# Optimization experiments

Measured on AMD Instinct MI355X. Metric: run time of the kernel, lower is better.

Reference implementation:

```python
import jax, jax.numpy as jnp
import numpy as np

NUM_EMBEDDINGS = 1024
EMBEDDING_DIM = 256
COMMITMENT_COST = 0.25


def setup_inputs() -> dict:
    key = jax.random.key(0)
    k1, k2 = jax.random.split(key)
    x = jax.random.normal(k1, (64, EMBEDDING_DIM, 32, 32), dtype=jnp.float32)
    # nn.init.uniform_(weight, -1/K, 1/K)
    lim = 1.0 / NUM_EMBEDDINGS
    codebook = jax.random.uniform(k2, (NUM_EMBEDDINGS, EMBEDDING_DIM),
                                  dtype=jnp.float32, minval=-lim, maxval=lim)
    return {"x": x, "codebook": codebook}


def reference(x, codebook):
    # x: [B, D, H, W], codebook: [K, D]
    B, D, H, W = x.shape
    xf = jnp.moveaxis(x, 1, -1).reshape(-1, D)  # [N, D], N = B*H*W
    # Squared L2 distances via expansion (same argmin as vector_norm of diff),
    # avoids materializing the [N, K, D] difference tensor.
    d2 = (
        jnp.sum(xf * xf, axis=-1, keepdims=True)          # [N, 1]
        - 2.0 * jnp.einsum("nd,kd->nk", xf, codebook)      # [N, K]
        + jnp.sum(codebook * codebook, axis=-1)            # [K]
    )
    idx = jnp.argmin(d2, axis=-1)                          # [N]
    q = codebook[idx].reshape(B, H, W, D)                  # gather + reshape
    q = jnp.moveaxis(q, -1, 1)                             # [B, D, H, W]

    codebook_loss = jnp.mean((jax.lax.stop_gradient(x) - q) ** 2)
    commitment_loss = COMMITMENT_COST * jnp.mean((x - jax.lax.stop_gradient(q)) ** 2)
    vq_loss = codebook_loss + commitment_loss

    # Straight-through estimator
    quantized = x + jax.lax.stop_gradient(q - x)
    return quantized, vq_loss
```

## Files before the change

### kernel.cpp

```cpp
#include <hip/hip_runtime.h>

#define BATCH 64
#define DIM 256
#define HW 1024
#define N_POS 65536
#define K_CODES 1024
#define NTOT 16777216

typedef __bf16 bf16x8 __attribute__((ext_vector_type(8)));
typedef float f32x4 __attribute__((ext_vector_type(4)));

__device__ inline unsigned short f2bf(float f) {
    unsigned int u = __builtin_bit_cast(unsigned int, f);
    unsigned int r = u + 0x7FFFu + ((u >> 16) & 1u);
    return (unsigned short)(r >> 16);
}
__device__ inline float bf2f(unsigned short u) {
    unsigned int x = ((unsigned int)u) << 16;
    return __builtin_bit_cast(float, x);
}

__global__ void cbprep_kernel(const float* __restrict__ cb, unsigned short* __restrict__ cbt,
                              float* __restrict__ cnorm) {
    const int wv = threadIdx.x >> 6, lane = threadIdx.x & 63;
    const int k = blockIdx.x * 4 + wv;
    const float4 v = *reinterpret_cast<const float4*>(cb + (size_t)k * DIM + lane * 4);
    ushort4 pk;
    pk.x = f2bf(v.x); pk.y = f2bf(v.y); pk.z = f2bf(v.z); pk.w = f2bf(v.w);
    *reinterpret_cast<ushort4*>(cbt + (size_t)k * DIM + lane * 4) = pk;
    const float f0 = bf2f(pk.x), f1 = bf2f(pk.y), f2 = bf2f(pk.z), f3 = bf2f(pk.w);
    float s = f0 * f0 + f1 * f1 + f2 * f2 + f3 * f3;
    #pragma unroll
    for (int off = 32; off; off >>= 1) s += __shfl_xor(s, off);
    if (lane == 0) cnorm[k] = 0.5f * s;
}

__global__ __launch_bounds__(256) void transpose_kernel(
        const float* __restrict__ x, unsigned short* __restrict__ xt) {
    __shared__ unsigned char ts[64 * 512];
    const int tid = threadIdx.x;
    const int b  = blockIdx.x >> 4;
    const int p0 = (blockIdx.x & 15) << 6;
    const float* xb = x + (size_t)b * (DIM * HW) + p0;
    const int p4 = tid & 15;
    const int dh = tid >> 4;
    #pragma unroll
    for (int dp = 0; dp < 8; ++dp) {
        const int d0 = dp * 32 + dh * 2;
        const float4 v0 = *reinterpret_cast<const float4*>(xb + (size_t)d0 * HW + p4 * 4);
        const float4 v1 = *reinterpret_cast<const float4*>(xb + (size_t)(d0 + 1) * HW + p4 * 4);
        const float a0[4] = {v0.x, v0.y, v0.z, v0.w};
        const float a1[4] = {v1.x, v1.y, v1.z, v1.w};
        #pragma unroll
        for (int e = 0; e < 4; ++e) {
            const int p = p4 * 4 + e;
            const unsigned int pk = (unsigned int)f2bf(a0[e]) | ((unsigned int)f2bf(a1[e]) << 16);
            const int col = (d0 * 2) ^ ((p & 7) << 4);
            *reinterpret_cast<unsigned int*>(&ts[p * 512 + col]) = pk;
        }
    }
    __syncthreads();
    const int ck = tid & 31;
    const int pr = tid >> 5;
    unsigned char* xt8 = (unsigned char*)xt;
    #pragma unroll
    for (int pp = 0; pp < 8; ++pp) {
        const int p = pp * 8 + pr;
        const uint4 v = *reinterpret_cast<const uint4*>(&ts[p * 512 + ((ck * 16) ^ ((p & 7) << 4))]);
        *reinterpret_cast<uint4*>(xt8 + (((size_t)(b * HW + p0 + p)) << 9) + ck * 16) = v;
    }
}

__global__ __launch_bounds__(256, 2) void score_kernel(
        const unsigned short* __restrict__ xt, const unsigned short* __restrict__ cbt,
        const float* __restrict__ cnorm, int* __restrict__ idx_out) {
    __shared__ unsigned char xs[64 * 1024];
    const int tid = threadIdx.x;
    const int l = tid & 63, w = tid >> 6;
    const int n0 = blockIdx.x * 128;
    const unsigned char* cbt8 = (const unsigned char*)cbt;

    {
        const unsigned char* xt8 = (const unsigned char*)xt;
        #pragma unroll
        for (int it = 0; it < 16; ++it) {
            const int X = w * 1024 + it * 4096 + l * 16;
            const int pos = X >> 9, col = X & 511;
            const unsigned char* src = xt8 + ((size_t)(n0 + pos) << 9) + (col ^ ((pos & 7) << 4));
            __builtin_amdgcn_global_load_lds(
                (const __attribute__((address_space(1))) void*)src,
                (__attribute__((address_space(3))) void*)(&xs[w * 1024 + it * 4096]),
                16, 0, 0);
        }
    }
    __syncthreads();

    const int wr = w >> 1, wc = w & 1;
    const int g = l >> 4, ln = l & 15;
    const int posbase = wr * 64;

    float bestv[16];
    int   besti[16];
    #pragma unroll
    for (int i = 0; i < 16; ++i) { bestv[i] = -3.0e38f; besti[i] = 0; }

    #pragma unroll 1
    for (int kt = 0; kt < 8; ++kt) {
        const int c0 = kt * 128 + wc * 64;
        f32x4 acc[4][4];
        #pragma unroll
        for (int mf = 0; mf < 4; ++mf)
            #pragma unroll
            for (int nf = 0; nf < 4; ++nf)
                acc[mf][nf] = (f32x4){0.f, 0.f, 0.f, 0.f};
        #pragma unroll 2
        for (int kk = 0; kk < 8; ++kk) {
            bf16x8 af[4], bfr[4];
            #pragma unroll
            for (int mf = 0; mf < 4; ++mf) {
                const int pos = posbase + mf * 16 + ln;
                const int colb = (kk * 64 + g * 16) ^ ((pos & 7) << 4);
                af[mf] = *reinterpret_cast<const bf16x8*>(&xs[pos * 512 + colb]);
            }
            #pragma unroll
            for (int nf = 0; nf < 4; ++nf) {
                const int code = c0 + nf * 16 + ln;
                bfr[nf] = *reinterpret_cast<const bf16x8*>(
                    cbt8 + ((size_t)code << 9) + kk * 64 + g * 16);
            }
            #pragma unroll
            for (int mf = 0; mf < 4; ++mf)
                #pragma unroll
                for (int nf = 0; nf < 4; ++nf)
                    acc[mf][nf] = __builtin_amdgcn_mfma_f32_16x16x32_bf16(
                        af[mf], bfr[nf], acc[mf][nf], 0, 0, 0);
        }
        #pragma unroll
        for (int nf = 0; nf < 4; ++nf) {
            const int k = c0 + nf * 16 + ln;
            const float cn = cnorm[k];
            #pragma unroll
            for (int mf = 0; mf < 4; ++mf)
                #pragma unroll
                for (int r = 0; r < 4; ++r) {
                    const float s = acc[mf][nf][r] - cn;
                    const int slot = mf * 4 + r;
                    if (s > bestv[slot]) { bestv[slot] = s; besti[slot] = k; }
                }
        }
    }

    #pragma unroll
    for (int off = 1; off < 16; off <<= 1) {
        #pragma unroll
        for (int slot = 0; slot < 16; ++slot) {
            const float ov = __shfl_xor(bestv[slot], off);
            const int   oi = __shfl_xor(besti[slot], off);
            if (ov > bestv[slot] || (ov == bestv[slot] && oi < besti[slot])) {
                bestv[slot] = ov; besti[slot] = oi;
            }
        }
    }
    __syncthreads();
    float* rv = (float*)xs;
    int*   ri = (int*)(xs + 512);
    if (wc == 1 && ln == 0) {
        #pragma unroll
        for (int mf = 0; mf < 4; ++mf)
            #pragma unroll
            for (int r = 0; r < 4; ++r) {
                const int pl = mf * 16 + g * 4 + r;
                rv[wr * 64 + pl] = bestv[mf * 4 + r];
                ri[wr * 64 + pl] = besti[mf * 4 + r];
            }
    }
    __syncthreads();
    if (wc == 0 && ln == 0) {
        #pragma unroll
        for (int mf = 0; mf < 4; ++mf)
            #pragma unroll
            for (int r = 0; r < 4; ++r) {
                const int pl = mf * 16 + g * 4 + r;
                float bv = bestv[mf * 4 + r];
                int   bi = besti[mf * 4 + r];
                const float ov = rv[wr * 64 + pl];
                const int   oi = ri[wr * 64 + pl];
                if (ov > bv || (ov == bv && oi < bi)) { bv = ov; bi = oi; }
                idx_out[n0 + wr * 64 + pl] = bi;
            }
    }
}

__global__ __launch_bounds__(256) void quantize_kernel(
        const float* __restrict__ x, const float* __restrict__ cb,
        const int* __restrict__ idx, float* __restrict__ out,
        float* __restrict__ partial) {
    const int blk = blockIdx.x;
    const int n0 = blk * 64;
    const int b  = n0 >> 10;
    const int p0 = n0 & 1023;
    const int lane = threadIdx.x & 63;
    const int w    = threadIdx.x >> 6;
    const int ci = idx[n0 + lane];
    const float4* cbrow4 = reinterpret_cast<const float4*>(cb + (size_t)ci * DIM);
    const size_t base = (size_t)b * DIM * HW + p0 + lane;

    float s = 0.0f;
    #pragma unroll
    for (int dq = 0; dq < 16; ++dq) {
        const float4 cq = cbrow4[w * 16 + dq];
        const int dbase = w * 64 + dq * 4;
        const float qv[4] = {cq.x, cq.y, cq.z, cq.w};
        #pragma unroll
        for (int e = 0; e < 4; ++e) {
            const int d = dbase + e;
            const float xv = x[base + (size_t)d * HW];
            out[base + (size_t)d * HW] = qv[e];
            const float diff = xv - qv[e];
            s = fmaf(diff, diff, s);
        }
    }
    #pragma unroll
    for (int off = 32; off; off >>= 1) s += __shfl_xor(s, off);
    __shared__ float wsum[4];
    if (lane == 0) wsum[w] = s;
    __syncthreads();
    if (threadIdx.x == 0) partial[blk] = wsum[0] + wsum[1] + wsum[2] + wsum[3];
}

__global__ void finalize_kernel(const float* __restrict__ partial, float* __restrict__ out_loss) {
    float s = 0.0f;
    for (int i = threadIdx.x; i < 1024; i += 256) s += partial[i];
    #pragma unroll
    for (int off = 32; off; off >>= 1) s += __shfl_xor(s, off);
    __shared__ float wsum[4];
    if ((threadIdx.x & 63) == 0) wsum[threadIdx.x >> 6] = s;
    __syncthreads();
    if (threadIdx.x == 0)
        out_loss[0] = 1.25f * (wsum[0] + wsum[1] + wsum[2] + wsum[3]) / (float)NTOT;
}

extern "C" void kernel_launch(void* const* d_in, const int* in_sizes, int n_in,
                              void* d_out, int out_size, void* d_ws, size_t ws_size,
                              hipStream_t stream) {
    const float* x  = (const float*)d_in[0];
    const float* cb = (const float*)d_in[1];
    float* out = (float*)d_out;

    unsigned short* xt  = (unsigned short*)d_out;
    unsigned short* cbt = xt + (size_t)N_POS * DIM;
    int*   idx     = (int*)d_ws;
    float* partial = (float*)((char*)d_ws + 262144);
    float* cnorm   = (float*)((char*)d_ws + 262144 + 4096);

    cbprep_kernel  <<<dim3(256),  dim3(256), 0, stream>>>(cb, cbt, cnorm);
    transpose_kernel<<<dim3(1024), dim3(256), 0, stream>>>(x, xt);
    score_kernel   <<<dim3(512),  dim3(256), 0, stream>>>(xt, cbt, cnorm, idx);
    quantize_kernel<<<dim3(1024), dim3(256), 0, stream>>>(x, cb, idx, out, partial);
    finalize_kernel<<<dim3(1),    dim3(256), 0, stream>>>(partial, out + NTOT);
}
```

Measured before the change: 215.5 us.

## Restructure score warp tiling with packed argmax and vectorize quantize kernel

The score kernel now gives each wave all 128 positions and a disjoint 256-code slice. Codebook fragments are double-buffered from global memory, and the bias (1 - cnorm) is folded into the accumulator initialisation. Argmin becomes an unsigned max over float bits whose low 10 bits are replaced by the inverted code index, merged across waves with LDS atomicMax. This cuts compare/select work but truncates the score mantissa, so near-ties may resolve differently. The quantize kernel is regridded to 256 blocks with float4 loads and stores over four positions per thread, and finalize is shrunk to match.

Result: slower. 267.3 us (+24.0%).

```diff
diff --git a/kernel.cpp b/kernel.cpp
--- a/kernel.cpp
+++ b/kernel.cpp
@@ -19,6 +19,7 @@
     unsigned int x = ((unsigned int)u) << 16;
     return __builtin_bit_cast(float, x);
 }
+__device__ inline unsigned umax2(unsigned a, unsigned b) { return a > b ? a : b; }
 
 __global__ void cbprep_kernel(const float* __restrict__ cb, unsigned short* __restrict__ cbt,
                               float* __restrict__ cnorm) {
@@ -71,6 +72,29 @@
     }
 }
 
+#define BSTEP(KK, BCUR, BNXT)                                                      \
+    {                                                                              \
+        bf16x8 af[8];                                                              \
+        _Pragma("unroll")                                                          \
+        for (int mf = 0; mf < 8; ++mf) {                                           \
+            const int pos = mf * 16 + ln;                                          \
+            const int colb = (((KK) * 64 + g * 16)) ^ ((ln & 7) << 4);             \
+            af[mf] = *reinterpret_cast<const bf16x8*>(&xs[pos * 512 + colb]);      \
+        }                                                                          \
+        if ((KK) + 1 < 8) {                                                        \
+            _Pragma("unroll")                                                      \
+            for (int nf = 0; nf < 4; ++nf)                                         \
+                BNXT[nf] = *reinterpret_cast<const bf16x8*>(                       \
+                    cbt8 + ((size_t)(c0 + nf * 16 + ln) << 9) + ((KK) + 1) * 64 + g * 16); \
+        }                                                                          \
+        _Pragma("unroll")                                                          \
+        for (int mf = 0; mf < 8; ++mf)                                             \
+            _Pragma("unroll")                                                      \
+            for (int nf = 0; nf < 4; ++nf)                                         \
+                acc[mf][nf] = __builtin_amdgcn_mfma_f32_16x16x32_bf16(             \
+                    af[mf], BCUR[nf], acc[mf][nf], 0, 0, 0);                       \
+    }
+
 __global__ __launch_bounds__(256, 2) void score_kernel(
         const unsigned short* __restrict__ xt, const unsigned short* __restrict__ cbt,
         const float* __restrict__ cnorm, int* __restrict__ idx_out) {
@@ -95,100 +119,74 @@
     }
     __syncthreads();
 
-    const int wr = w >> 1, wc = w & 1;
     const int g = l >> 4, ln = l & 15;
-    const int posbase = wr * 64;
-
-    float bestv[16];
-    int   besti[16];
-    #pragma unroll
-    for (int i = 0; i < 16; ++i) { bestv[i] = -3.0e38f; besti[i] = 0; }
+
+    unsigned bestp[32];
+    #pragma unroll
+    for (int i = 0; i < 32; ++i) bestp[i] = 0u;
 
     #pragma unroll 1
-    for (int kt = 0; kt < 8; ++kt) {
-        const int c0 = kt * 128 + wc * 64;
-        f32x4 acc[4][4];
-        #pragma unroll
-        for (int mf = 0; mf < 4; ++mf)
+    for (int kt = 0; kt < 4; ++kt) {
+        const int c0 = w * 256 + kt * 64;
+        float adj[4]; unsigned iv[4];
+        #pragma unroll
+        for (int nf = 0; nf < 4; ++nf) {
+            const int k = c0 + nf * 16 + ln;
+            adj[nf] = 1.0f - cnorm[k];
+            iv[nf] = (unsigned)(1023 - k) & 1023u;
+        }
+        f32x4 acc[8][4];
+        #pragma unroll
+        for (int mf = 0; mf < 8; ++mf)
             #pragma unroll
             for (int nf = 0; nf < 4; ++nf)
-                acc[mf][nf] = (f32x4){0.f, 0.f, 0.f, 0.f};
-        #pragma unroll 2
-        for (int kk = 0; kk < 8; ++kk) {
-            bf16x8 af[4], bfr[4];
+                acc[mf][nf] = (f32x4){adj[nf], adj[nf], adj[nf], adj[nf]};
+
+        bf16x8 bA[4], bB[4];
+        #pragma unroll
+        for (int nf = 0; nf < 4; ++nf)
+            bA[nf] = *reinterpret_cast<const bf16x8*>(
+                cbt8 + ((size_t)(c0 + nf * 16 + ln) << 9) + g * 16);
+
+        BSTEP(0, bA, bB) BSTEP(1, bB, bA)
+        BSTEP(2, bA, bB) BSTEP(3, bB, bA)
+        BSTEP(4, bA, bB) BSTEP(5, bB, bA)
+        BSTEP(6, bA, bB) BSTEP(7, bB, bA)
+
+        #pragma unroll
+        for (int mf = 0; mf < 8; ++mf)
             #pragma unroll
-            for (int mf = 0; mf < 4; ++mf) {
-                const int pos = posbase + mf * 16 + ln;
-                const int colb = (kk * 64 + g * 16) ^ ((pos & 7) << 4);
-                af[mf] = *reinterpret_cast<const bf16x8*>(&xs[pos * 512 + colb]);
-            }
-            #pragma unroll
-            for (int nf = 0; nf < 4; ++nf) {
-                const int code = c0 + nf * 16 + ln;
-                bfr[nf] = *reinterpret_cast<const bf16x8*>(
-                    cbt8 + ((size_t)code << 9) + kk * 64 + g * 16);
-            }
-            #pragma unroll
-            for (int mf = 0; mf < 4; ++mf)
+            for (int r = 0; r < 4; ++r) {
+                unsigned c[4];
                 #pragma unroll
                 for (int nf = 0; nf < 4; ++nf)
-                    acc[mf][nf] = __builtin_amdgcn_mfma_f32_16x16x32_bf16(
-                        af[mf], bfr[nf], acc[mf][nf], 0, 0, 0);
-        }
-        #pragma unroll
-        for (int nf = 0; nf < 4; ++nf) {
-            const int k = c0 + nf * 16 + ln;
-            const float cn = cnorm[k];
+                    c[nf] = (__builtin_bit_cast(unsigned, acc[mf][nf][r]) & 0xFFFFFC00u) | iv[nf];
+                unsigned b = bestp[mf * 4 + r];
+                b = umax2(b, umax2(umax2(c[0], c[1]), umax2(c[2], c[3])));
+                bestp[mf * 4 + r] = b;
+            }
+    }
+
+    #pragma unroll
+    for (int off = 1; off < 16; off <<= 1) {
+        #pragma unroll
+        for (int s = 0; s < 32; ++s)
+            bestp[s] = umax2(bestp[s], (unsigned)__shfl_xor((int)bestp[s], off));
+    }
+
+    __syncthreads();
+    unsigned* merged = (unsigned*)xs;
+    if (tid < 128) merged[tid] = 0u;
+    __syncthreads();
+    if (ln == 0) {
+        #pragma unroll
+        for (int mf = 0; mf < 8; ++mf)
             #pragma unroll
-            for (int mf = 0; mf < 4; ++mf)
-                #pragma unroll
-                for (int r = 0; r < 4; ++r) {
-                    const float s = acc[mf][nf][r] - cn;
-                    const int slot = mf * 4 + r;
-                    if (s > bestv[slot]) { bestv[slot] = s; besti[slot] = k; }
-                }
-        }
-    }
-
-    #pragma unroll
-    for (int off = 1; off < 16; off <<= 1) {
-        #pragma unroll
-        for (int slot = 0; slot < 16; ++slot) {
-            const float ov = __shfl_xor(bestv[slot], off);
-            const int   oi = __shfl_xor(besti[slot], off);
-            if (ov > bestv[slot] || (ov == bestv[slot] && oi < besti[slot])) {
-                bestv[slot] = ov; besti[slot] = oi;
-            }
-        }
-    }
-    __syncthreads();
-    float* rv = (float*)xs;
-    int*   ri = (int*)(xs + 512);
-    if (wc == 1 && ln == 0) {
-        #pragma unroll
-        for (int mf = 0; mf < 4; ++mf)
-            #pragma unroll
-            for (int r = 0; r < 4; ++r) {
-                const int pl = mf * 16 + g * 4 + r;
-                rv[wr * 64 + pl] = bestv[mf * 4 + r];
-                ri[wr * 64 + pl] = besti[mf * 4 + r];
-            }
-    }
-    __syncthreads();
-    if (wc == 0 && ln == 0) {
-        #pragma unroll
-        for (int mf = 0; mf < 4; ++mf)
-            #pragma unroll
-            for (int r = 0; r < 4; ++r) {
-                const int pl = mf * 16 + g * 4 + r;
-                float bv = bestv[mf * 4 + r];
-                int   bi = besti[mf * 4 + r];
-                const float ov = rv[wr * 64 + pl];
-                const int   oi = ri[wr * 64 + pl];
-                if (ov > bv || (ov == bv && oi < bi)) { bv = ov; bi = oi; }
-                idx_out[n0 + wr * 64 + pl] = bi;
-            }
-    }
+            for (int r = 0; r < 4; ++r)
+                atomicMax(&merged[mf * 16 + g * 4 + r], bestp[mf * 4 + r]);
+    }
+    __syncthreads();
+    if (tid < 128) idx_out[n0 + tid] = 1023 - (int)(merged[tid] & 1023u);
 }
 
 __global__ __launch_bounds__(256) void quantize_kernel(
@@ -196,41 +194,46 @@
         const int* __restrict__ idx, float* __restrict__ out,
         float* __restrict__ partial) {
     const int blk = blockIdx.x;
-    const int n0 = blk * 64;
-    const int b  = n0 >> 10;
-    const int p0 = n0 & 1023;
-    const int lane = threadIdx.x & 63;
-    const int w    = threadIdx.x >> 6;
-    const int ci = idx[n0 + lane];
-    const float4* cbrow4 = reinterpret_cast<const float4*>(cb + (size_t)ci * DIM);
-    const size_t base = (size_t)b * DIM * HW + p0 + lane;
+    const int b  = blk >> 2;
+    const int d0 = (blk & 3) * 64;
+    const int tid = threadIdx.x;
+    const int4 ci = *reinterpret_cast<const int4*>(&idx[b * HW + tid * 4]);
+    const int cia[4] = {ci.x, ci.y, ci.z, ci.w};
+    const size_t xbase = (size_t)b * (DIM * HW) + tid * 4;
 
     float s = 0.0f;
-    #pragma unroll
+    #pragma unroll 4
     for (int dq = 0; dq < 16; ++dq) {
-        const float4 cq = cbrow4[w * 16 + dq];
-        const int dbase = w * 64 + dq * 4;
-        const float qv[4] = {cq.x, cq.y, cq.z, cq.w};
-        #pragma unroll
-        for (int e = 0; e < 4; ++e) {
-            const int d = dbase + e;
-            const float xv = x[base + (size_t)d * HW];
-            out[base + (size_t)d * HW] = qv[e];
-            const float diff = xv - qv[e];
-            s = fmaf(diff, diff, s);
+        const int dd = d0 + dq * 4;
+        float4 xv[4], cv[4];
+        #pragma unroll
+        for (int j = 0; j < 4; ++j)
+            xv[j] = *reinterpret_cast<const float4*>(&x[xbase + (size_t)(dd + j) * HW]);
+        #pragma unroll
+        for (int e = 0; e < 4; ++e)
+            cv[e] = *reinterpret_cast<const float4*>(&cb[(size_t)cia[e] * DIM + dd]);
+        #pragma unroll
+        for (int j = 0; j < 4; ++j) {
+            const float q0 = (&cv[0].x)[j], q1 = (&cv[1].x)[j],
+                        q2 = (&cv[2].x)[j], q3 = (&cv[3].x)[j];
+            float4 ov = {q0, q1, q2, q3};
+            *reinterpret_cast<float4*>(&out[xbase + (size_t)(dd + j) * HW]) = ov;
+            const float e0 = xv[j].x - q0, e1 = xv[j].y - q1,
+                        e2 = xv[j].z - q2, e3 = xv[j].w - q3;
+            s = fmaf(e0, e0, s); s = fmaf(e1, e1, s);
+            s = fmaf(e2, e2, s); s = fmaf(e3, e3, s);
         }
     }
     #pragma unroll
     for (int off = 32; off; off >>= 1) s += __shfl_xor(s, off);
     __shared__ float wsum[4];
-    if (lane == 0) wsum[w] = s;
-    __syncthreads();
-    if (threadIdx.x == 0) partial[blk] = wsum[0] + wsum[1] + wsum[2] + wsum[3];
+    if ((tid & 63) == 0) wsum[tid >> 6] = s;
+    __syncthreads();
+    if (tid == 0) partial[blk] = wsum[0] + wsum[1] + wsum[2] + wsum[3];
 }
 
 __global__ void finalize_kernel(const float* __restrict__ partial, float* __restrict__ out_loss) {
-    float s = 0.0f;
-    for (int i = threadIdx.x; i < 1024; i += 256) s += partial[i];
+    float s = (threadIdx.x < 256) ? partial[threadIdx.x] : 0.0f;
     #pragma unroll
     for (int off = 32; off; off >>= 1) s += __shfl_xor(s, off);
     __shared__ float wsum[4];
@@ -253,9 +256,9 @@
     float* partial = (float*)((char*)d_ws + 262144);
     float* cnorm   = (float*)((char*)d_ws + 262144 + 4096);
 
-    cbprep_kernel  <<<dim3(256),  dim3(256), 0, stream>>>(cb, cbt, cnorm);
+    cbprep_kernel   <<<dim3(256),  dim3(256), 0, stream>>>(cb, cbt, cnorm);
     transpose_kernel<<<dim3(1024), dim3(256), 0, stream>>>(x, xt);
-    score_kernel   <<<dim3(512),  dim3(256), 0, stream>>>(xt, cbt, cnorm, idx);
-    quantize_kernel<<<dim3(1024), dim3(256), 0, stream>>>(x, cb, idx, out, partial);
-    finalize_kernel<<<dim3(1),    dim3(256), 0, stream>>>(partial, out + NTOT);
-}
+    score_kernel    <<<dim3(512),  dim3(256), 0, stream>>>(xt, cbt, cnorm, idx);
+    quantize_kernel <<<dim3(256),  dim3(256), 0, stream>>>(x, cb, idx, out, partial);
+    finalize_kernel <<<dim3(1),    dim3(256), 0, stream>>>(partial, out + NTOT);
+}
```
